# Optimization experiments

Hardware: AMD Instinct MI355X
Metric: run time of the kernel (lower is better)

## Reference

```python
import jax, jax.numpy as jnp
import numpy as np

HIDDEN = 1024
HEADS = 16
HEAD = HIDDEN // HEADS
B, S = 4, 2048


def setup_inputs() -> dict:
    key = jax.random.key(0)
    ks = jax.random.split(key, 12)
    sc = 1.0 / np.sqrt(HIDDEN)
    return {
        "query": jax.random.normal(ks[0], (B, S, HIDDEN), jnp.float32),
        "key_in": jax.random.normal(ks[1], (B, S, HIDDEN), jnp.float32),
        "value": jax.random.normal(ks[2], (B, S, HIDDEN), jnp.float32),
        "mask": jax.random.randint(ks[3], (B, S, S), 0, 2, jnp.int32),
        "w_q": jax.random.uniform(ks[4], (HIDDEN, HIDDEN), jnp.float32, -sc, sc),
        "b_q": jax.random.uniform(ks[5], (HIDDEN,), jnp.float32, -sc, sc),
        "w_k": jax.random.uniform(ks[6], (HIDDEN, HIDDEN), jnp.float32, -sc, sc),
        "b_k": jax.random.uniform(ks[7], (HIDDEN,), jnp.float32, -sc, sc),
        "w_v": jax.random.uniform(ks[8], (HIDDEN, HIDDEN), jnp.float32, -sc, sc),
        "b_v": jax.random.uniform(ks[9], (HIDDEN,), jnp.float32, -sc, sc),
    }


def _split_heads(x):
    # [B, S, H*D] -> [B, H, S, D]
    b, s, _ = x.shape
    return x.reshape(b, s, HEADS, HEAD).transpose(0, 2, 1, 3)


def reference(query, key_in, value, mask, w_q, b_q, w_k, b_k, w_v, b_v):
    # torch Linear: x @ W.T + b
    Q = _split_heads(query @ w_q.T + b_q)
    K = _split_heads(key_in @ w_k.T + b_k)
    V = _split_heads(value @ w_v.T + b_v)
    scale = 1.0 / np.sqrt(HEAD).astype(np.float32)
    scores = jnp.einsum("bhqd,bhkd->bhqk", Q, K) * scale
    # mask broadcast over heads; masked_fill where mask == 0
    scores = jnp.where(mask[:, None, :, :] == 0, jnp.float32(-1e9), scores)
    attn = jax.nn.softmax(scores, axis=-1)
    ctx = jnp.einsum("bhqk,bhkd->bhqd", attn, V)
    ctx = ctx.transpose(0, 2, 1, 3).reshape(query.shape[0], -1, HIDDEN)
    return (ctx, attn)
```

## Files before the change

### kernel.cpp

```cpp
#include <hip/hip_runtime.h>
#include <hip/hip_bf16.h>
#include <cstdint>
#include <cstddef>

typedef __attribute__((ext_vector_type(4))) float f32x4;
typedef __attribute__((ext_vector_type(8))) short s16x8;
typedef __attribute__((ext_vector_type(8))) unsigned short u16x8;
typedef __attribute__((ext_vector_type(4))) unsigned short u16x4;
typedef unsigned short ushort_t;
typedef unsigned long long u64;

#define MFMA_BF16(a, b, c) __builtin_amdgcn_mfma_f32_16x16x32_bf16((a), (b), (c), 0, 0, 0)

constexpr int BATCH  = 4;
constexpr int SEQ    = 2048;
constexpr int NHEAD  = 16;
constexpr int HEADD  = 64;
constexpr int HID    = 1024;
constexpr int BH     = BATCH * NHEAD;

#define QSCALE 0.180336880091961f

__device__ __forceinline__ ushort_t f2bf(float f) {
  return __builtin_bit_cast(ushort_t, __float2bfloat16(f));
}

__device__ __forceinline__ int ps_off(int q, int k) {
  return q * 136 + ((((k >> 3) ^ ((q >> 3) & 7)) & 15) << 3) + (k & 7);
}

__global__ __launch_bounds__(256, 2) void proj_fused_kernel(
    const float* __restrict__ q_in, const float* __restrict__ k_in,
    const float* __restrict__ v_in,
    const float* __restrict__ w_q, const float* __restrict__ b_q,
    const float* __restrict__ w_k, const float* __restrict__ b_k,
    const float* __restrict__ w_v, const float* __restrict__ b_v,
    ushort_t* __restrict__ Qp, ushort_t* __restrict__ Kp,
    ushort_t* __restrict__ Vp,
    const int* __restrict__ mask, u64* __restrict__ pm) {
  const int z = blockIdx.z;
  if (z == 3) {
    const int nwords = BATCH * SEQ * SEQ / 64;
    const int lane = threadIdx.x & 63;
    int wid = (blockIdx.y * gridDim.x + blockIdx.x) * 4 + (threadIdx.x >> 6);
    const int step = gridDim.x * gridDim.y * 4;
    for (; wid < nwords; wid += step) {
      int mv = mask[(size_t)wid * 64 + lane];
      u64 bits = __ballot(mv != 0);
      if (lane == 0) pm[wid] = bits;
    }
    return;
  }
  const float* X    = (z == 0) ? q_in : (z == 1) ? k_in : v_in;
  const float* W    = (z == 0) ? w_q : (z == 1) ? w_k : w_v;
  const float* bias = (z == 0) ? b_q : (z == 1) ? b_k : b_v;
  const float scale = (z == 0) ? QSCALE : 1.0f;

  __shared__ ushort_t As[128 * 72];
  __shared__ ushort_t Bs[128 * 72];
  const int tid  = threadIdx.x;
  const int lane = tid & 63;
  const int wave = tid >> 6;
  const int wr = wave >> 1, wc = wave & 1;
  const int lo = lane & 15, hi = lane >> 4;
  const int mb = blockIdx.y, nb = blockIdx.x;

  const int srow = tid >> 4;
  const int scol = (tid & 15) * 4;

  f32x4 acc[4][4];
#pragma unroll
  for (int i = 0; i < 4; i++)
#pragma unroll
    for (int j = 0; j < 4; j++) acc[i][j] = (f32x4){0.f, 0.f, 0.f, 0.f};

  const float* xa = X + (size_t)(mb * 128 + srow) * HID + scol;
  const float* xb = W + (size_t)(nb * 128 + srow) * HID + scol;

  for (int k0 = 0; k0 < HID; k0 += 64) {
#pragma unroll
    for (int rr = 0; rr < 128; rr += 16) {
      float4 av = *(const float4*)(xa + (size_t)rr * HID + k0);
      float4 bv = *(const float4*)(xb + (size_t)rr * HID + k0);
      u16x4 a4 = {f2bf(av.x), f2bf(av.y), f2bf(av.z), f2bf(av.w)};
      u16x4 b4 = {f2bf(bv.x), f2bf(bv.y), f2bf(bv.z), f2bf(bv.w)};
      *(u16x4*)(&As[(srow + rr) * 72 + scol]) = a4;
      *(u16x4*)(&Bs[(srow + rr) * 72 + scol]) = b4;
    }
    __syncthreads();
#pragma unroll
    for (int kk = 0; kk < 2; kk++) {
      const int ko = kk * 32 + hi * 8;
      s16x8 af[4], bf[4];
#pragma unroll
      for (int i = 0; i < 4; i++)
        af[i] = *(const s16x8*)(&As[(wr * 64 + i * 16 + lo) * 72 + ko]);
#pragma unroll
      for (int j = 0; j < 4; j++)
        bf[j] = *(const s16x8*)(&Bs[(wc * 64 + j * 16 + lo) * 72 + ko]);
#pragma unroll
      for (int i = 0; i < 4; i++)
#pragma unroll
        for (int j = 0; j < 4; j++)
          acc[i][j] = MFMA_BF16(af[i], bf[j], acc[i][j]);
    }
    __syncthreads();
  }
  if (z != 2) {
    ushort_t* out = (z == 0) ? Qp : Kp;
#pragma unroll
    for (int j = 0; j < 4; j++) {
      const int n = nb * 128 + wc * 64 + j * 16 + lo;
      const float bvn = bias[n];
      const int h = n >> 6, d = n & 63;
#pragma unroll
      for (int i = 0; i < 4; i++) {
        const int m0 = mb * 128 + wr * 64 + i * 16 + hi * 4;
#pragma unroll
        for (int r = 0; r < 4; r++) {
          const int m = m0 + r;
          const int b = m >> 11, s = m & 2047;
          float v = (acc[i][j][r] + bvn) * scale;
          out[(((size_t)(b * NHEAD + h) * SEQ) + s) * HEADD + d] = f2bf(v);
        }
      }
    }
  } else {
#pragma unroll
    for (int j = 0; j < 4; j++) {
      const int n = nb * 128 + wc * 64 + j * 16 + lo;
      const float bvn = bias[n];
      const int h = n >> 6, d = n & 63;
#pragma unroll
      for (int i = 0; i < 4; i++) {
        const int m0 = mb * 128 + wr * 64 + i * 16 + hi * 4;
        const int b = m0 >> 11, s0 = m0 & 2047;
        u16x4 pk = {f2bf(acc[i][j][0] + bvn), f2bf(acc[i][j][1] + bvn),
                    f2bf(acc[i][j][2] + bvn), f2bf(acc[i][j][3] + bvn)};
        *(u16x4*)(Vp + ((size_t)(b * NHEAD + h) * HEADD + d) * SEQ + s0) = pk;
      }
    }
  }
}

__global__ __launch_bounds__(256, 2) void fused_attn_kernel(
    const ushort_t* __restrict__ Qp, const ushort_t* __restrict__ Kp,
    const ushort_t* __restrict__ Vtg, const u64* __restrict__ pm,
    float* __restrict__ attn, float* __restrict__ ctx) {
  extern __shared__ ushort_t smem[];
  ushort_t* Vt = smem;
  ushort_t* Ps = smem + 8704;

  const int tid  = threadIdx.x;
  const int lane = tid & 63, wave = tid >> 6;
  const int lo = lane & 15, hi = lane >> 4;

  const int f  = blockIdx.x;
  const int wg = (f & 7) * 128 + (f >> 3);
  const int bh = wg >> 4, qb = wg & 15;
  const int b = bh >> 4, h = bh & 15;

  const ushort_t* Qg = Qp + ((size_t)bh * SEQ + qb * 128 + wave * 32) * HEADD;
  s16x8 aq[2][2];
#pragma unroll
  for (int i = 0; i < 2; i++)
#pragma unroll
    for (int kk = 0; kk < 2; kk++)
      aq[i][kk] = *(const s16x8*)(Qg + (size_t)(i * 16 + lo) * HEADD + kk * 32 + hi * 8);

  const ushort_t* Kg = Kp + (size_t)bh * SEQ * HEADD;
  const ushort_t* Vg = Vtg + (size_t)bh * HEADD * SEQ;
  const u64* pmb = pm + (size_t)b * SEQ * 32;
  const int q0 = qb * 128 + wave * 32;

  float lrun[2][4];
#pragma unroll
  for (int i = 0; i < 2; i++)
#pragma unroll
    for (int r = 0; r < 4; r++) lrun[i][r] = 0.f;
  f32x4 pacc[2][4];
#pragma unroll
  for (int i = 0; i < 2; i++)
#pragma unroll
    for (int jd = 0; jd < 4; jd++) pacc[i][jd] = (f32x4){0.f, 0.f, 0.f, 0.f};

  const int vr16 = tid >> 4;
  const int vc8  = (tid & 15) * 8;

  for (int kt = 0; kt < SEQ / 128; kt++) {
    u16x8 vreg[4];
#pragma unroll
    for (int it = 0; it < 4; it++)
      vreg[it] = *(const u16x8*)(Vg + (size_t)(it * 16 + vr16) * SEQ + kt * 128 + vc8);

    f32x4 sacc[2][8];
#pragma unroll
    for (int i = 0; i < 2; i++)
#pragma unroll
      for (int j = 0; j < 8; j++) sacc[i][j] = (f32x4){0.f, 0.f, 0.f, 0.f};
#pragma unroll
    for (int j = 0; j < 8; j++) {
      const ushort_t* kr = Kg + (size_t)(kt * 128 + j * 16 + lo) * HEADD + hi * 8;
      s16x8 b0 = *(const s16x8*)(kr);
      s16x8 b1 = *(const s16x8*)(kr + 32);
      sacc[0][j] = MFMA_BF16(aq[0][0], b0, sacc[0][j]);
      sacc[1][j] = MFMA_BF16(aq[1][0], b0, sacc[1][j]);
      sacc[0][j] = MFMA_BF16(aq[0][1], b1, sacc[0][j]);
      sacc[1][j] = MFMA_BF16(aq[1][1], b1, sacc[1][j]);
    }

#pragma unroll
    for (int it = 0; it < 4; it++)
      *(u16x8*)(&Vt[(it * 16 + vr16) * 136 + vc8]) = vreg[it];

#pragma unroll
    for (int i = 0; i < 2; i++)
#pragma unroll
      for (int r = 0; r < 4; r++) {
        const int q = q0 + i * 16 + hi * 4 + r;
        const u64* pw = pmb + (size_t)q * 32 + kt * 2;
        u64 s0 = pw[0] >> lo, s1 = pw[1] >> lo;
        const int prow = wave * 32 + i * 16 + hi * 4 + r;
        float tsum = 0.f;
#pragma unroll
        for (int j = 0; j < 8; j++) {
          unsigned bit = (unsigned)((j < 4 ? (s0 >> (j * 16)) : (s1 >> ((j - 4) * 16))) & 1ull);
          float s = bit ? sacc[i][j][r] : -1e30f;
          float ev = __builtin_amdgcn_exp2f(s);
          tsum += ev;
          Ps[ps_off(prow, j * 16 + lo)] = f2bf(ev);
        }
        lrun[i][r] += tsum;
      }
    __syncthreads();

#pragma unroll
    for (int kkp = 0; kkp < 4; kkp++) {
      const int ko = kkp * 32 + hi * 8;
      s16x8 ap0 = *(const s16x8*)(&Ps[ps_off(wave * 32 + lo, ko)]);
      s16x8 ap1 = *(const s16x8*)(&Ps[ps_off(wave * 32 + 16 + lo, ko)]);
#pragma unroll
      for (int jd = 0; jd < 4; jd++) {
        s16x8 bv = *(const s16x8*)(&Vt[(jd * 16 + lo) * 136 + ko]);
        pacc[0][jd] = MFMA_BF16(ap0, bv, pacc[0][jd]);
        pacc[1][jd] = MFMA_BF16(ap1, bv, pacc[1][jd]);
      }
    }
    __syncthreads();
  }

  float il[2][4], mi[2][4];
#pragma unroll
  for (int i = 0; i < 2; i++)
#pragma unroll
    for (int r = 0; r < 4; r++) {
      float l = lrun[i][r];
#pragma unroll
      for (int off = 1; off < 16; off <<= 1) l += __shfl_xor(l, off);
      il[i][r] = 1.0f / l;
      mi[i][r] = __builtin_amdgcn_logf(l);
    }
#pragma unroll
  for (int i = 0; i < 2; i++)
#pragma unroll
    for (int jd = 0; jd < 4; jd++)
#pragma unroll
      for (int r = 0; r < 4; r++) {
        const int q = q0 + i * 16 + hi * 4 + r;
        ctx[((size_t)b * SEQ + q) * HID + h * HEADD + jd * 16 + lo] =
            pacc[i][jd][r] * il[i][r];
      }

  for (int kt = 0; kt < SEQ / 128; kt++) {
    f32x4 sacc[2][8];
#pragma unroll
    for (int i = 0; i < 2; i++)
#pragma unroll
      for (int j = 0; j < 8; j++) sacc[i][j] = (f32x4){0.f, 0.f, 0.f, 0.f};
#pragma unroll
    for (int j = 0; j < 8; j++) {
      const ushort_t* kr = Kg + (size_t)(kt * 128 + j * 16 + lo) * HEADD + hi * 8;
      s16x8 b0 = *(const s16x8*)(kr);
      s16x8 b1 = *(const s16x8*)(kr + 32);
      sacc[0][j] = MFMA_BF16(aq[0][0], b0, sacc[0][j]);
      sacc[1][j] = MFMA_BF16(aq[1][0], b0, sacc[1][j]);
      sacc[0][j] = MFMA_BF16(aq[0][1], b1, sacc[0][j]);
      sacc[1][j] = MFMA_BF16(aq[1][1], b1, sacc[1][j]);
    }
#pragma unroll
    for (int i = 0; i < 2; i++)
#pragma unroll
      for (int r = 0; r < 4; r++) {
        const int q = q0 + i * 16 + hi * 4 + r;
        const u64* pw = pmb + (size_t)q * 32 + kt * 2;
        u64 s0 = pw[0] >> lo, s1 = pw[1] >> lo;
        const size_t abase = ((size_t)bh * SEQ + q) * SEQ + (size_t)kt * 128;
        const float miv = mi[i][r];
#pragma unroll
        for (int j = 0; j < 8; j++) {
          unsigned bit = (unsigned)((j < 4 ? (s0 >> (j * 16)) : (s1 >> ((j - 4) * 16))) & 1ull);
          float s = bit ? sacc[i][j][r] : -1e30f;
          attn[abase + j * 16 + lo] = __builtin_amdgcn_exp2f(s - miv);
        }
      }
  }
}

extern "C" void kernel_launch(void* const* d_in, const int* in_sizes, int n_in,
                              void* d_out, int out_size, void* d_ws, size_t ws_size,
                              hipStream_t stream) {
  const float* query  = (const float*)d_in[0];
  const float* key_in = (const float*)d_in[1];
  const float* value  = (const float*)d_in[2];
  const int*   mask   = (const int*)d_in[3];
  const float* w_q = (const float*)d_in[4];
  const float* b_q = (const float*)d_in[5];
  const float* w_k = (const float*)d_in[6];
  const float* b_k = (const float*)d_in[7];
  const float* w_v = (const float*)d_in[8];
  const float* b_v = (const float*)d_in[9];

  char* ws = (char*)d_ws;
  const size_t proj_elems = (size_t)BATCH * NHEAD * SEQ * HEADD;
  ushort_t* Qp = (ushort_t*)ws;
  ushort_t* Kp = Qp + proj_elems;
  ushort_t* Vp = Kp + proj_elems;
  u64* pmask   = (u64*)(ws + 3 * proj_elems * sizeof(ushort_t));

  float* ctx  = (float*)d_out;
  float* attn = ctx + (size_t)BATCH * SEQ * HID;

  proj_fused_kernel<<<dim3(HID / 128, (BATCH * SEQ) / 128, 4), dim3(256), 0, stream>>>(
      query, key_in, value, w_q, b_q, w_k, b_k, w_v, b_v, Qp, Kp, Vp, mask, pmask);

  const size_t lds_attn = (8704 + 17408) * sizeof(ushort_t);
  fused_attn_kernel<<<dim3(BH * (SEQ / 128)), dim3(256), lds_attn, stream>>>(
      Qp, Kp, Vp, pmask, attn, ctx);
}
```

Baseline: 798.9 us.

## Split fused attention into PV kernel and separate attn-probability store kernel

The single fused kernel, which ran QK twice (once for the softmax denominator and PV, once to write attn), becomes two kernels. The first computes ctx and writes the per-row log-sum to a workspace. The second recomputes QK with 32x32x16 MFMAs and streams the normalized, masked probabilities to attn. The first kernel's QK is also split into two halves to cut live registers, with the occupancy hint raised to 3. The aim is higher occupancy and better overlap of the large attn write, at the cost of an extra launch and a round trip through global memory for the row statistics.

```diff
diff --git a/kernel.cpp b/kernel.cpp
--- a/kernel.cpp
+++ b/kernel.cpp
@@ -3,14 +3,16 @@
 #include <cstdint>
 #include <cstddef>
 
-typedef __attribute__((ext_vector_type(4))) float f32x4;
-typedef __attribute__((ext_vector_type(8))) short s16x8;
-typedef __attribute__((ext_vector_type(8))) unsigned short u16x8;
-typedef __attribute__((ext_vector_type(4))) unsigned short u16x4;
+typedef __attribute__((ext_vector_type(4)))  float f32x4;
+typedef __attribute__((ext_vector_type(16))) float f32x16;
+typedef __attribute__((ext_vector_type(8)))  short s16x8;
+typedef __attribute__((ext_vector_type(8)))  unsigned short u16x8;
+typedef __attribute__((ext_vector_type(4)))  unsigned short u16x4;
 typedef unsigned short ushort_t;
 typedef unsigned long long u64;
 
-#define MFMA_BF16(a, b, c) __builtin_amdgcn_mfma_f32_16x16x32_bf16((a), (b), (c), 0, 0, 0)
+#define MFMA_BF16(a, b, c)   __builtin_amdgcn_mfma_f32_16x16x32_bf16((a), (b), (c), 0, 0, 0)
+#define MFMA32_BF16(a, b, c) __builtin_amdgcn_mfma_f32_32x32x16_bf16((a), (b), (c), 0, 0, 0)
 
 constexpr int BATCH  = 4;
 constexpr int SEQ    = 2048;
@@ -143,10 +145,10 @@
   }
 }
 
-__global__ __launch_bounds__(256, 2) void fused_attn_kernel(
+__global__ __launch_bounds__(256, 3) void attn_pv_kernel(
     const ushort_t* __restrict__ Qp, const ushort_t* __restrict__ Kp,
     const ushort_t* __restrict__ Vtg, const u64* __restrict__ pm,
-    float* __restrict__ attn, float* __restrict__ ctx) {
+    float* __restrict__ mi_ws, float* __restrict__ ctx) {
   extern __shared__ ushort_t smem[];
   ushort_t* Vt = smem;
   ushort_t* Ps = smem + 8704;
@@ -193,45 +195,48 @@
     for (int it = 0; it < 4; it++)
       vreg[it] = *(const u16x8*)(Vg + (size_t)(it * 16 + vr16) * SEQ + kt * 128 + vc8);
 
-    f32x4 sacc[2][8];
-#pragma unroll
-    for (int i = 0; i < 2; i++)
-#pragma unroll
-      for (int j = 0; j < 8; j++) sacc[i][j] = (f32x4){0.f, 0.f, 0.f, 0.f};
-#pragma unroll
-    for (int j = 0; j < 8; j++) {
-      const ushort_t* kr = Kg + (size_t)(kt * 128 + j * 16 + lo) * HEADD + hi * 8;
-      s16x8 b0 = *(const s16x8*)(kr);
-      s16x8 b1 = *(const s16x8*)(kr + 32);
-      sacc[0][j] = MFMA_BF16(aq[0][0], b0, sacc[0][j]);
-      sacc[1][j] = MFMA_BF16(aq[1][0], b0, sacc[1][j]);
-      sacc[0][j] = MFMA_BF16(aq[0][1], b1, sacc[0][j]);
-      sacc[1][j] = MFMA_BF16(aq[1][1], b1, sacc[1][j]);
-    }
-
-#pragma unroll
-    for (int it = 0; it < 4; it++)
-      *(u16x8*)(&Vt[(it * 16 + vr16) * 136 + vc8]) = vreg[it];
-
-#pragma unroll
-    for (int i = 0; i < 2; i++)
-#pragma unroll
-      for (int r = 0; r < 4; r++) {
-        const int q = q0 + i * 16 + hi * 4 + r;
-        const u64* pw = pmb + (size_t)q * 32 + kt * 2;
-        u64 s0 = pw[0] >> lo, s1 = pw[1] >> lo;
-        const int prow = wave * 32 + i * 16 + hi * 4 + r;
-        float tsum = 0.f;
-#pragma unroll
-        for (int j = 0; j < 8; j++) {
-          unsigned bit = (unsigned)((j < 4 ? (s0 >> (j * 16)) : (s1 >> ((j - 4) * 16))) & 1ull);
-          float s = bit ? sacc[i][j][r] : -1e30f;
-          float ev = __builtin_amdgcn_exp2f(s);
-          tsum += ev;
-          Ps[ps_off(prow, j * 16 + lo)] = f2bf(ev);
+#pragma unroll
+    for (int half = 0; half < 2; half++) {
+      f32x4 sacc[2][4];
+#pragma unroll
+      for (int i = 0; i < 2; i++)
+#pragma unroll
+        for (int j = 0; j < 4; j++) sacc[i][j] = (f32x4){0.f, 0.f, 0.f, 0.f};
+#pragma unroll
+      for (int j4 = 0; j4 < 4; j4++) {
+        const int j = half * 4 + j4;
+        const ushort_t* kr = Kg + (size_t)(kt * 128 + j * 16 + lo) * HEADD + hi * 8;
+        s16x8 b0 = *(const s16x8*)(kr);
+        s16x8 b1 = *(const s16x8*)(kr + 32);
+        sacc[0][j4] = MFMA_BF16(aq[0][0], b0, sacc[0][j4]);
+        sacc[1][j4] = MFMA_BF16(aq[1][0], b0, sacc[1][j4]);
+        sacc[0][j4] = MFMA_BF16(aq[0][1], b1, sacc[0][j4]);
+        sacc[1][j4] = MFMA_BF16(aq[1][1], b1, sacc[1][j4]);
+      }
+      if (half == 0) {
+#pragma unroll
+        for (int it = 0; it < 4; it++)
+          *(u16x8*)(&Vt[(it * 16 + vr16) * 136 + vc8]) = vreg[it];
+      }
+#pragma unroll
+      for (int i = 0; i < 2; i++)
+#pragma unroll
+        for (int r = 0; r < 4; r++) {
+          const int q = q0 + i * 16 + hi * 4 + r;
+          u64 s0 = pmb[(size_t)q * 32 + kt * 2 + half] >> lo;
+          const int prow = wave * 32 + i * 16 + hi * 4 + r;
+          float tsum = 0.f;
+#pragma unroll
+          for (int j4 = 0; j4 < 4; j4++) {
+            unsigned bit = (unsigned)((s0 >> (j4 * 16)) & 1ull);
+            float s = bit ? sacc[i][j4][r] : -1e30f;
+            float ev = __builtin_amdgcn_exp2f(s);
+            tsum += ev;
+            Ps[ps_off(prow, half * 64 + j4 * 16 + lo)] = f2bf(ev);
+          }
+          lrun[i][r] += tsum;
         }
-        lrun[i][r] += tsum;
-      }
+    }
     __syncthreads();
 
 #pragma unroll
@@ -249,7 +254,7 @@
     __syncthreads();
   }
 
-  float il[2][4], mi[2][4];
+  float il[2][4], miv[2][4];
 #pragma unroll
   for (int i = 0; i < 2; i++)
 #pragma unroll
@@ -257,8 +262,8 @@
       float l = lrun[i][r];
 #pragma unroll
       for (int off = 1; off < 16; off <<= 1) l += __shfl_xor(l, off);
-      il[i][r] = 1.0f / l;
-      mi[i][r] = __builtin_amdgcn_logf(l);
+      il[i][r]  = 1.0f / l;
+      miv[i][r] = __builtin_amdgcn_logf(l);
     }
 #pragma unroll
   for (int i = 0; i < 2; i++)
@@ -270,39 +275,66 @@
         ctx[((size_t)b * SEQ + q) * HID + h * HEADD + jd * 16 + lo] =
             pacc[i][jd][r] * il[i][r];
       }
-
-  for (int kt = 0; kt < SEQ / 128; kt++) {
-    f32x4 sacc[2][8];
+  if (lo == 0) {
 #pragma unroll
     for (int i = 0; i < 2; i++)
 #pragma unroll
-      for (int j = 0; j < 8; j++) sacc[i][j] = (f32x4){0.f, 0.f, 0.f, 0.f};
-#pragma unroll
-    for (int j = 0; j < 8; j++) {
-      const ushort_t* kr = Kg + (size_t)(kt * 128 + j * 16 + lo) * HEADD + hi * 8;
-      s16x8 b0 = *(const s16x8*)(kr);
-      s16x8 b1 = *(const s16x8*)(kr + 32);
-      sacc[0][j] = MFMA_BF16(aq[0][0], b0, sacc[0][j]);
-      sacc[1][j] = MFMA_BF16(aq[1][0], b0, sacc[1][j]);
-      sacc[0][j] = MFMA_BF16(aq[0][1], b1, sacc[0][j]);
-      sacc[1][j] = MFMA_BF16(aq[1][1], b1, sacc[1][j]);
-    }
-#pragma unroll
-    for (int i = 0; i < 2; i++)
-#pragma unroll
-      for (int r = 0; r < 4; r++) {
-        const int q = q0 + i * 16 + hi * 4 + r;
-        const u64* pw = pmb + (size_t)q * 32 + kt * 2;
-        u64 s0 = pw[0] >> lo, s1 = pw[1] >> lo;
-        const size_t abase = ((size_t)bh * SEQ + q) * SEQ + (size_t)kt * 128;
-        const float miv = mi[i][r];
-#pragma unroll
-        for (int j = 0; j < 8; j++) {
-          unsigned bit = (unsigned)((j < 4 ? (s0 >> (j * 16)) : (s1 >> ((j - 4) * 16))) & 1ull);
-          float s = bit ? sacc[i][j][r] : -1e30f;
-          attn[abase + j * 16 + lo] = __builtin_amdgcn_exp2f(s - miv);
-        }
-      }
+      for (int r = 0; r < 4; r++)
+        mi_ws[bh * SEQ + q0 + i * 16 + hi * 4 + r] = miv[i][r];
+  }
+}
+
+__global__ __launch_bounds__(256, 4) void attn_store_kernel(
+    const ushort_t* __restrict__ Qp, const ushort_t* __restrict__ Kp,
+    const u64* __restrict__ pm, const float* __restrict__ mi_ws,
+    float* __restrict__ attn) {
+  const int tid  = threadIdx.x;
+  const int lane = tid & 63, wave = tid >> 6;
+  const int l31 = lane & 31, h32 = lane >> 5;
+
+  const int f  = blockIdx.x;
+  const int wg = (f & 7) * 128 + (f >> 3);
+  const int bh = wg >> 4, qb = wg & 15;
+  const int b = bh >> 4;
+  const int q0w = qb * 128 + wave * 32;
+
+  const ushort_t* Qg = Qp + (size_t)bh * SEQ * HEADD;
+  const ushort_t* Kg = Kp + (size_t)bh * SEQ * HEADD;
+
+  s16x8 aq[4];
+#pragma unroll
+  for (int mf = 0; mf < 4; mf++)
+    aq[mf] = *(const s16x8*)(Qg + (size_t)(q0w + l31) * HEADD + mf * 16 + h32 * 8);
+
+  int qr[16];
+  float mi[16];
+#pragma unroll
+  for (int r = 0; r < 16; r++) {
+    qr[r] = q0w + (r & 3) + 8 * (r >> 2) + 4 * h32;
+    mi[r] = mi_ws[bh * SEQ + qr[r]];
+  }
+  const unsigned* pm32 = (const unsigned*)(pm + (size_t)b * SEQ * 32);
+  float* ab = attn + (size_t)bh * SEQ * SEQ;
+
+  for (int kc = 0; kc < SEQ / 32; kc++) {
+    s16x8 bk[4];
+#pragma unroll
+    for (int mf = 0; mf < 4; mf++)
+      bk[mf] = *(const s16x8*)(Kg + (size_t)(kc * 32 + l31) * HEADD + mf * 16 + h32 * 8);
+    f32x16 sacc;
+#pragma unroll
+    for (int t = 0; t < 16; t++) sacc[t] = 0.f;
+    sacc = MFMA32_BF16(aq[0], bk[0], sacc);
+    sacc = MFMA32_BF16(aq[1], bk[1], sacc);
+    sacc = MFMA32_BF16(aq[2], bk[2], sacc);
+    sacc = MFMA32_BF16(aq[3], bk[3], sacc);
+#pragma unroll
+    for (int r = 0; r < 16; r++) {
+      unsigned mw = pm32[(size_t)qr[r] * 64 + kc];
+      float e = __builtin_amdgcn_exp2f(sacc[r] - mi[r]);
+      e = ((mw >> l31) & 1u) ? e : 0.f;
+      ab[(size_t)qr[r] * SEQ + kc * 32 + l31] = e;
+    }
   }
 }
 
@@ -326,6 +358,7 @@
   ushort_t* Kp = Qp + proj_elems;
   ushort_t* Vp = Kp + proj_elems;
   u64* pmask   = (u64*)(ws + 3 * proj_elems * sizeof(ushort_t));
+  float* mi_ws = (float*)(pmask + (size_t)BATCH * SEQ * SEQ / 64);
 
   float* ctx  = (float*)d_out;
   float* attn = ctx + (size_t)BATCH * SEQ * HID;
@@ -333,7 +366,10 @@
   proj_fused_kernel<<<dim3(HID / 128, (BATCH * SEQ) / 128, 4), dim3(256), 0, stream>>>(
       query, key_in, value, w_q, b_q, w_k, b_k, w_v, b_v, Qp, Kp, Vp, mask, pmask);
 
-  const size_t lds_attn = (8704 + 17408) * sizeof(ushort_t);
-  fused_attn_kernel<<<dim3(BH * (SEQ / 128)), dim3(256), lds_attn, stream>>>(
-      Qp, Kp, Vp, pmask, attn, ctx);
-}
+  const size_t lds_pv = (8704 + 17408) * sizeof(ushort_t);
+  attn_pv_kernel<<<dim3(BH * (SEQ / 128)), dim3(256), lds_pv, stream>>>(
+      Qp, Kp, Vp, pmask, mi_ws, ctx);
+
+  attn_store_kernel<<<dim3(BH * (SEQ / 128)), dim3(256), 0, stream>>>(
+      Qp, Kp, pmask, mi_ws, attn);
+}
```

After: 886.8 us. 1.11x slower.

## Halve attention query tile to 64 rows per block for higher occupancy

Applied to the files above, without the earlier changes.

Each block now covers 64 query rows (16 per wave) instead of 128, which doubles the grid and halves LDS for the P buffer. Per-wave register arrays shrink, and launch bounds rise to three blocks per CU. The cost is that every K tile and V tile is loaded and QK^T is recomputed twice as often per query, because each K/V load now serves half as many rows.

```diff
diff --git a/kernel.cpp b/kernel.cpp
--- a/kernel.cpp
+++ b/kernel.cpp
@@ -3,10 +3,10 @@
 #include <cstdint>
 #include <cstddef>
 
-typedef __attribute__((ext_vector_type(4))) float f32x4;
-typedef __attribute__((ext_vector_type(8))) short s16x8;
-typedef __attribute__((ext_vector_type(8))) unsigned short u16x8;
-typedef __attribute__((ext_vector_type(4))) unsigned short u16x4;
+typedef __attribute__((ext_vector_type(4)))  float f32x4;
+typedef __attribute__((ext_vector_type(8)))  short s16x8;
+typedef __attribute__((ext_vector_type(8)))  unsigned short u16x8;
+typedef __attribute__((ext_vector_type(4)))  unsigned short u16x4;
 typedef unsigned short ushort_t;
 typedef unsigned long long u64;
 
@@ -18,6 +18,7 @@
 constexpr int HEADD  = 64;
 constexpr int HID    = 1024;
 constexpr int BH     = BATCH * NHEAD;
+constexpr int QBLK   = 64;
 
 #define QSCALE 0.180336880091961f
 
@@ -143,7 +144,7 @@
   }
 }
 
-__global__ __launch_bounds__(256, 2) void fused_attn_kernel(
+__global__ __launch_bounds__(256, 3) void fused_attn_kernel(
     const ushort_t* __restrict__ Qp, const ushort_t* __restrict__ Kp,
     const ushort_t* __restrict__ Vtg, const u64* __restrict__ pm,
     float* __restrict__ attn, float* __restrict__ ctx) {
@@ -156,33 +157,25 @@
   const int lo = lane & 15, hi = lane >> 4;
 
   const int f  = blockIdx.x;
-  const int wg = (f & 7) * 128 + (f >> 3);
-  const int bh = wg >> 4, qb = wg & 15;
+  const int wg = (f & 7) * 256 + (f >> 3);
+  const int bh = wg >> 5, qb = wg & 31;
   const int b = bh >> 4, h = bh & 15;
 
-  const ushort_t* Qg = Qp + ((size_t)bh * SEQ + qb * 128 + wave * 32) * HEADD;
-  s16x8 aq[2][2];
-#pragma unroll
-  for (int i = 0; i < 2; i++)
-#pragma unroll
-    for (int kk = 0; kk < 2; kk++)
-      aq[i][kk] = *(const s16x8*)(Qg + (size_t)(i * 16 + lo) * HEADD + kk * 32 + hi * 8);
+  const ushort_t* Qg = Qp + ((size_t)bh * SEQ + qb * QBLK + wave * 16) * HEADD;
+  s16x8 aq[2];
+#pragma unroll
+  for (int kk = 0; kk < 2; kk++)
+    aq[kk] = *(const s16x8*)(Qg + (size_t)lo * HEADD + kk * 32 + hi * 8);
 
   const ushort_t* Kg = Kp + (size_t)bh * SEQ * HEADD;
   const ushort_t* Vg = Vtg + (size_t)bh * HEADD * SEQ;
   const u64* pmb = pm + (size_t)b * SEQ * 32;
-  const int q0 = qb * 128 + wave * 32;
-
-  float lrun[2][4];
-#pragma unroll
-  for (int i = 0; i < 2; i++)
-#pragma unroll
-    for (int r = 0; r < 4; r++) lrun[i][r] = 0.f;
-  f32x4 pacc[2][4];
-#pragma unroll
-  for (int i = 0; i < 2; i++)
-#pragma unroll
-    for (int jd = 0; jd < 4; jd++) pacc[i][jd] = (f32x4){0.f, 0.f, 0.f, 0.f};
+  const int q0 = qb * QBLK + wave * 16;
+
+  float lrun[4] = {0.f, 0.f, 0.f, 0.f};
+  f32x4 pacc[4];
+#pragma unroll
+  for (int jd = 0; jd < 4; jd++) pacc[jd] = (f32x4){0.f, 0.f, 0.f, 0.f};
 
   const int vr16 = tid >> 4;
   const int vc8  = (tid & 15) * 8;
@@ -193,20 +186,16 @@
     for (int it = 0; it < 4; it++)
       vreg[it] = *(const u16x8*)(Vg + (size_t)(it * 16 + vr16) * SEQ + kt * 128 + vc8);
 
-    f32x4 sacc[2][8];
-#pragma unroll
-    for (int i = 0; i < 2; i++)
-#pragma unroll
-      for (int j = 0; j < 8; j++) sacc[i][j] = (f32x4){0.f, 0.f, 0.f, 0.f};
+    f32x4 sacc[8];
+#pragma unroll
+    for (int j = 0; j < 8; j++) sacc[j] = (f32x4){0.f, 0.f, 0.f, 0.f};
 #pragma unroll
     for (int j = 0; j < 8; j++) {
       const ushort_t* kr = Kg + (size_t)(kt * 128 + j * 16 + lo) * HEADD + hi * 8;
       s16x8 b0 = *(const s16x8*)(kr);
       s16x8 b1 = *(const s16x8*)(kr + 32);
-      sacc[0][j] = MFMA_BF16(aq[0][0], b0, sacc[0][j]);
-      sacc[1][j] = MFMA_BF16(aq[1][0], b0, sacc[1][j]);
-      sacc[0][j] = MFMA_BF16(aq[0][1], b1, sacc[0][j]);
-      sacc[1][j] = MFMA_BF16(aq[1][1], b1, sacc[1][j]);
+      sacc[j] = MFMA_BF16(aq[0], b0, sacc[j]);
+      sacc[j] = MFMA_BF16(aq[1], b1, sacc[j]);
     }
 
 #pragma unroll
@@ -214,95 +203,81 @@
       *(u16x8*)(&Vt[(it * 16 + vr16) * 136 + vc8]) = vreg[it];
 
 #pragma unroll
-    for (int i = 0; i < 2; i++)
-#pragma unroll
-      for (int r = 0; r < 4; r++) {
-        const int q = q0 + i * 16 + hi * 4 + r;
-        const u64* pw = pmb + (size_t)q * 32 + kt * 2;
-        u64 s0 = pw[0] >> lo, s1 = pw[1] >> lo;
-        const int prow = wave * 32 + i * 16 + hi * 4 + r;
-        float tsum = 0.f;
-#pragma unroll
-        for (int j = 0; j < 8; j++) {
-          unsigned bit = (unsigned)((j < 4 ? (s0 >> (j * 16)) : (s1 >> ((j - 4) * 16))) & 1ull);
-          float s = bit ? sacc[i][j][r] : -1e30f;
-          float ev = __builtin_amdgcn_exp2f(s);
-          tsum += ev;
-          Ps[ps_off(prow, j * 16 + lo)] = f2bf(ev);
-        }
-        lrun[i][r] += tsum;
-      }
+    for (int r = 0; r < 4; r++) {
+      const int q = q0 + hi * 4 + r;
+      const u64* pw = pmb + (size_t)q * 32 + kt * 2;
+      u64 s0 = pw[0] >> lo, s1 = pw[1] >> lo;
+      const int prow = wave * 16 + hi * 4 + r;
+      float tsum = 0.f;
+#pragma unroll
+      for (int j = 0; j < 8; j++) {
+        unsigned bit = (unsigned)((j < 4 ? (s0 >> (j * 16)) : (s1 >> ((j - 4) * 16))) & 1ull);
+        float s = bit ? sacc[j][r] : -1e30f;
+        float ev = __builtin_amdgcn_exp2f(s);
+        tsum += ev;
+        Ps[ps_off(prow, j * 16 + lo)] = f2bf(ev);
+      }
+      lrun[r] += tsum;
+    }
     __syncthreads();
 
 #pragma unroll
     for (int kkp = 0; kkp < 4; kkp++) {
       const int ko = kkp * 32 + hi * 8;
-      s16x8 ap0 = *(const s16x8*)(&Ps[ps_off(wave * 32 + lo, ko)]);
-      s16x8 ap1 = *(const s16x8*)(&Ps[ps_off(wave * 32 + 16 + lo, ko)]);
+      s16x8 ap = *(const s16x8*)(&Ps[ps_off(wave * 16 + lo, ko)]);
 #pragma unroll
       for (int jd = 0; jd < 4; jd++) {
         s16x8 bv = *(const s16x8*)(&Vt[(jd * 16 + lo) * 136 + ko]);
-        pacc[0][jd] = MFMA_BF16(ap0, bv, pacc[0][jd]);
-        pacc[1][jd] = MFMA_BF16(ap1, bv, pacc[1][jd]);
+        pacc[jd] = MFMA_BF16(ap, bv, pacc[jd]);
       }
     }
     __syncthreads();
   }
 
-  float il[2][4], mi[2][4];
-#pragma unroll
-  for (int i = 0; i < 2; i++)
+  float il[4], mi[4];
+#pragma unroll
+  for (int r = 0; r < 4; r++) {
+    float l = lrun[r];
+#pragma unroll
+    for (int off = 1; off < 16; off <<= 1) l += __shfl_xor(l, off);
+    il[r] = 1.0f / l;
+    mi[r] = __builtin_amdgcn_logf(l);
+  }
+#pragma unroll
+  for (int jd = 0; jd < 4; jd++)
 #pragma unroll
     for (int r = 0; r < 4; r++) {
-      float l = lrun[i][r];
-#pragma unroll
-      for (int off = 1; off < 16; off <<= 1) l += __shfl_xor(l, off);
-      il[i][r] = 1.0f / l;
-      mi[i][r] = __builtin_amdgcn_logf(l);
-    }
-#pragma unroll
-  for (int i = 0; i < 2; i++)
-#pragma unroll
-    for (int jd = 0; jd < 4; jd++)
-#pragma unroll
-      for (int r = 0; r < 4; r++) {
-        const int q = q0 + i * 16 + hi * 4 + r;
-        ctx[((size_t)b * SEQ + q) * HID + h * HEADD + jd * 16 + lo] =
-            pacc[i][jd][r] * il[i][r];
-      }
+      const int q = q0 + hi * 4 + r;
+      ctx[((size_t)b * SEQ + q) * HID + h * HEADD + jd * 16 + lo] =
+          pacc[jd][r] * il[r];
+    }
 
   for (int kt = 0; kt < SEQ / 128; kt++) {
-    f32x4 sacc[2][8];
-#pragma unroll
-    for (int i = 0; i < 2; i++)
-#pragma unroll
-      for (int j = 0; j < 8; j++) sacc[i][j] = (f32x4){0.f, 0.f, 0.f, 0.f};
+    f32x4 sacc[8];
+#pragma unroll
+    for (int j = 0; j < 8; j++) sacc[j] = (f32x4){0.f, 0.f, 0.f, 0.f};
 #pragma unroll
     for (int j = 0; j < 8; j++) {
       const ushort_t* kr = Kg + (size_t)(kt * 128 + j * 16 + lo) * HEADD + hi * 8;
       s16x8 b0 = *(const s16x8*)(kr);
       s16x8 b1 = *(const s16x8*)(kr + 32);
-      sacc[0][j] = MFMA_BF16(aq[0][0], b0, sacc[0][j]);
-      sacc[1][j] = MFMA_BF16(aq[1][0], b0, sacc[1][j]);
-      sacc[0][j] = MFMA_BF16(aq[0][1], b1, sacc[0][j]);
-      sacc[1][j] = MFMA_BF16(aq[1][1], b1, sacc[1][j]);
-    }
-#pragma unroll
-    for (int i = 0; i < 2; i++)
-#pragma unroll
-      for (int r = 0; r < 4; r++) {
-        const int q = q0 + i * 16 + hi * 4 + r;
-        const u64* pw = pmb + (size_t)q * 32 + kt * 2;
-        u64 s0 = pw[0] >> lo, s1 = pw[1] >> lo;
-        const size_t abase = ((size_t)bh * SEQ + q) * SEQ + (size_t)kt * 128;
-        const float miv = mi[i][r];
-#pragma unroll
-        for (int j = 0; j < 8; j++) {
-          unsigned bit = (unsigned)((j < 4 ? (s0 >> (j * 16)) : (s1 >> ((j - 4) * 16))) & 1ull);
-          float s = bit ? sacc[i][j][r] : -1e30f;
-          attn[abase + j * 16 + lo] = __builtin_amdgcn_exp2f(s - miv);
-        }
-      }
+      sacc[j] = MFMA_BF16(aq[0], b0, sacc[j]);
+      sacc[j] = MFMA_BF16(aq[1], b1, sacc[j]);
+    }
+#pragma unroll
+    for (int r = 0; r < 4; r++) {
+      const int q = q0 + hi * 4 + r;
+      const u64* pw = pmb + (size_t)q * 32 + kt * 2;
+      u64 s0 = pw[0] >> lo, s1 = pw[1] >> lo;
+      const size_t abase = ((size_t)bh * SEQ + q) * SEQ + (size_t)kt * 128;
+      const float miv = mi[r];
+#pragma unroll
+      for (int j = 0; j < 8; j++) {
+        unsigned bit = (unsigned)((j < 4 ? (s0 >> (j * 16)) : (s1 >> ((j - 4) * 16))) & 1ull);
+        float s = bit ? sacc[j][r] : -1e30f;
+        attn[abase + j * 16 + lo] = __builtin_amdgcn_exp2f(s - miv);
+      }
+    }
   }
 }
 
@@ -333,7 +308,7 @@
   proj_fused_kernel<<<dim3(HID / 128, (BATCH * SEQ) / 128, 4), dim3(256), 0, stream>>>(
       query, key_in, value, w_q, b_q, w_k, b_k, w_v, b_v, Qp, Kp, Vp, mask, pmask);
 
-  const size_t lds_attn = (8704 + 17408) * sizeof(ushort_t);
-  fused_attn_kernel<<<dim3(BH * (SEQ / 128)), dim3(256), lds_attn, stream>>>(
+  const size_t lds_attn = (8704 + 8704) * sizeof(ushort_t);
+  fused_attn_kernel<<<dim3(BH * (SEQ / QBLK)), dim3(256), lds_attn, stream>>>(
       Qp, Kp, Vp, pmask, attn, ctx);
 }
```

After: 932.9 us. 16.8% more time.
